# Performance work log

Hardware: AMD Instinct MI355X
Metric: run time of the kernel (lower is better)

## Reference

```python
import jax, jax.numpy as jnp
import numpy as np

B, N, F_IN, C_OUT = 128, 512, 2, 64
C_IN = F_IN + C_OUT           # 66, concat(input, state) feature dim
MLP_IN = (2 * 3 + 1) * C_IN   # order=2, support_len=3 -> 462


def _gcn(x, supports, W, b):
    """Diffusion conv: x [B,N,F]; for each support a, 2 diffusion orders."""
    outs = [x]
    for a in supports:
        x1 = jnp.einsum('bnf,nm->bmf', x, a)
        x2 = jnp.einsum('bnf,nm->bmf', x1, a)
        outs += [x1, x2]
    h = jnp.concatenate(outs, axis=2)  # [B, N, 7*F]
    return h @ W + b                   # Linear (dropout is eval-mode identity)


def setup_inputs() -> dict:
    key = jax.random.key(0)
    ks = jax.random.split(key, 12)
    return {
        'input': jax.random.normal(ks[0], (B, N, F_IN), dtype=jnp.float32),
        'state': jax.random.normal(ks[1], (B, N, C_OUT), dtype=jnp.float32),
        'A0':    jax.random.uniform(ks[2], (N, N), dtype=jnp.float32),
        'A1':    jax.random.uniform(ks[3], (N, N), dtype=jnp.float32),
        'nv1_1': jax.random.normal(ks[4], (N, 10), dtype=jnp.float32),
        'nv2_1': jax.random.normal(ks[5], (10, N), dtype=jnp.float32),
        'W1':    jax.random.normal(ks[6], (MLP_IN, 2 * C_OUT), dtype=jnp.float32) * 0.02,
        'b1':    jnp.zeros((2 * C_OUT,), dtype=jnp.float32),
        'nv1_2': jax.random.normal(ks[7], (N, 10), dtype=jnp.float32),
        'nv2_2': jax.random.normal(ks[8], (10, N), dtype=jnp.float32),
        'W2':    jax.random.normal(ks[9], (MLP_IN, C_OUT), dtype=jnp.float32) * 0.02,
        'b2':    jnp.zeros((C_OUT,), dtype=jnp.float32),
    }


def reference(input, state, A0, A1, nv1_1, nv2_1, W1, b1, nv1_2, nv2_2, W2, b2):
    c_out = state.shape[-1]
    # gcn_1: adaptive adjacency + diffusion conv, then sigmoid gating split into r,u
    adp1 = jax.nn.softmax(jax.nn.relu(nv1_1 @ nv2_1), axis=1)
    x = jnp.concatenate([input, state], axis=2)
    value = jax.nn.sigmoid(_gcn(x, [A0, A1, adp1], W1, b1))
    r, u = value[..., :c_out], value[..., c_out:]
    # gcn_2: candidate state
    adp2 = jax.nn.softmax(jax.nn.relu(nv1_2 @ nv2_2), axis=1)
    x2 = jnp.concatenate([input, r * state], axis=2)
    c = jnp.tanh(_gcn(x2, [A0, A1, adp2], W2, b2))
    return u * state + (1.0 - u) * c
```

## Files before the change

### kernel.cpp

```cpp
#include <hip/hip_runtime.h>
#include <math.h>

#define NN 512
#define BB 128
#define CIN 66
#define QQ (BB*CIN)
#define AN ((size_t)NN*NN)
#define HB 480
#define KTOT 480

typedef unsigned short ushort_t;
typedef __attribute__((ext_vector_type(8))) short short8;
typedef __attribute__((ext_vector_type(8))) unsigned short us8;
typedef __attribute__((ext_vector_type(4))) float f32x4;
typedef __attribute__((ext_vector_type(4))) unsigned short us4;

__device__ __forceinline__ ushort_t f2bf(float f) {
    unsigned u = __float_as_uint(f);
    u += 0x7FFF + ((u >> 16) & 1);
    return (ushort_t)(u >> 16);
}
__device__ __forceinline__ float bf2f(ushort_t h) {
    return __uint_as_float(((unsigned)h) << 16);
}
__device__ __forceinline__ void split_bf(float f, ushort_t& hi, ushort_t& lo) {
    hi = f2bf(f);
    lo = f2bf(f - bf2f(hi));
}
__device__ __forceinline__ void gload_lds16(const void* g, void* l) {
    __builtin_amdgcn_global_load_lds(
        (const __attribute__((address_space(1))) unsigned*)g,
        (__attribute__((address_space(3))) unsigned*)l, 16, 0, 0);
}

__global__ __launch_bounds__(512) void adp_kernel(const float* __restrict__ nv1,
                                                  const float* __restrict__ nv2,
                                                  float* __restrict__ adp) {
    int n = blockIdx.x;
    int m = threadIdx.x;
    float z = 0.f;
#pragma unroll
    for (int k = 0; k < 10; k++) z = fmaf(nv1[n * 10 + k], nv2[k * NN + m], z);
    z = fmaxf(z, 0.f);

    __shared__ float sred[8];
    int wid  = threadIdx.x >> 6;
    int lane = threadIdx.x & 63;

    float v = z;
#pragma unroll
    for (int off = 32; off; off >>= 1) v = fmaxf(v, __shfl_down(v, off, 64));
    if (lane == 0) sred[wid] = v;
    __syncthreads();
    float zmax = sred[0];
#pragma unroll
    for (int i = 1; i < 8; i++) zmax = fmaxf(zmax, sred[i]);

    float e = __expf(z - zmax);
    __syncthreads();
    v = e;
#pragma unroll
    for (int off = 32; off; off >>= 1) v += __shfl_down(v, off, 64);
    if (lane == 0) sred[wid] = v;
    __syncthreads();
    float tot = 0.f;
#pragma unroll
    for (int i = 0; i < 8; i++) tot += sred[i];

    adp[n * NN + m] = e / tot;
}

__global__ __launch_bounds__(256) void asplit_kernel(const float* __restrict__ A0,
                                                     const float* __restrict__ A1,
                                                     const float* __restrict__ P1,
                                                     const float* __restrict__ P2,
                                                     ushort_t* __restrict__ Ahi,
                                                     ushort_t* __restrict__ Alo) {
    __shared__ float t[32][33];
    int s = blockIdx.z;
    const float* src = (s == 0) ? A0 : (s == 1) ? A1 : (s == 2) ? P1 : P2;
    int m0 = blockIdx.x * 32, k0 = blockIdx.y * 32;
    int tx = threadIdx.x & 31, ty = threadIdx.x >> 5;
#pragma unroll
    for (int r = 0; r < 32; r += 8)
        t[ty + r][tx] = src[(size_t)(k0 + ty + r) * NN + m0 + tx];
    __syncthreads();
#pragma unroll
    for (int r = 0; r < 32; r += 8) {
        int m = m0 + ty + r, k = k0 + tx;
        float v = t[tx][ty + r];
        ushort_t h, l; split_bf(v, h, l);
        size_t o = ((size_t)s * NN + m) * NN + k;
        Ahi[o] = h; Alo[o] = l;
    }
}

template <int COUT>
__global__ __launch_bounds__(256) void wtprep_kernel(const float* __restrict__ W,
                                                     ushort_t* __restrict__ Wth,
                                                     ushort_t* __restrict__ Wtl) {
    int j = blockIdx.x;
    for (int k = threadIdx.x; k < KTOT; k += 256) {
        float v = (k < 462) ? W[(size_t)k * COUT + j] : 0.f;
        ushort_t h, l; split_bf(v, h, l);
        Wth[(size_t)j * KTOT + k] = h;
        Wtl[(size_t)j * KTOT + k] = l;
    }
}

__global__ __launch_bounds__(256) void buildx_kernel(const float* __restrict__ inp,
                                                     const float* __restrict__ st,
                                                     ushort_t* __restrict__ Hh,
                                                     ushort_t* __restrict__ Hl) {
    int b = blockIdx.y, n = blockIdx.x * 64 + (threadIdx.x & 63);
    int cg = threadIdx.x >> 6;
    size_t bn = (size_t)b * NN + n;
    for (int c = cg; c < CIN; c += 4) {
        float v = (c < 2) ? inp[bn * 2 + c] : st[bn * 64 + (c - 2)];
        ushort_t h, l; split_bf(v, h, l);
        Hh[((size_t)b * HB + c) * NN + n] = h;
        Hl[((size_t)b * HB + c) * NN + n] = l;
    }
}

template <int HOP>
__global__ __launch_bounds__(256) void diff_mfma(const ushort_t* __restrict__ Ahi,
                                                 const ushort_t* __restrict__ Alo,
                                                 ushort_t* Hh, ushort_t* Hl, int s2) {
    __shared__ ushort_t sAh[128 * 32];
    __shared__ ushort_t sAl[128 * 32];
    __shared__ ushort_t sXh[128 * 32];
    __shared__ ushort_t sXl[128 * 32];
    const int tid  = threadIdx.x;
    const int lane = tid & 63, w = tid >> 6;
    const int quad = lane >> 4, l15 = lane & 15;
    const int q0 = blockIdx.x * 128, m0 = blockIdx.y * 128;
    const int sz = blockIdx.z;
    const int sup = (sz < 2) ? sz : s2;
    const ushort_t* Ah = Ahi + (size_t)sup * AN;
    const ushort_t* Al = Alo + (size_t)sup * AN;
    const int roff_in = (HOP == 1) ? 0 : 66 + 132 * sz;
    const int wm = w & 1, wq = w >> 1;

    size_t aoff[2], xoff[2];
    int ldo[2];
#pragma unroll
    for (int p = 0; p < 2; p++) {
        int cid = p * 256 + tid;
        int row = cid >> 2, kk = (cid & 3) * 8;
        ldo[p]  = cid * 8;
        aoff[p] = (size_t)(m0 + row) * NN + kk;
        int q = q0 + row, b = q / 66, c = q - 66 * b;
        xoff[p] = ((size_t)b * HB + roff_in + c) * NN + kk;
    }

    f32x4 acc[4][4] = {};

    for (int k0 = 0; k0 < NN; k0 += 32) {
        __syncthreads();
#pragma unroll
        for (int p = 0; p < 2; p++) {
            gload_lds16(Ah + aoff[p] + k0, sAh + ldo[p]);
            gload_lds16(Al + aoff[p] + k0, sAl + ldo[p]);
            gload_lds16(Hh + xoff[p] + k0, sXh + ldo[p]);
            gload_lds16(Hl + xoff[p] + k0, sXl + ldo[p]);
        }
        __syncthreads();
        short8 ah[4], al[4], xh[4], xl[4];
#pragma unroll
        for (int t = 0; t < 4; t++) {
            int arow = wm * 64 + t * 16 + l15;
            int xrow = wq * 64 + t * 16 + l15;
            ah[t] = *(const short8*)&sAh[arow * 32 + quad * 8];
            al[t] = *(const short8*)&sAl[arow * 32 + quad * 8];
            xh[t] = *(const short8*)&sXh[xrow * 32 + quad * 8];
            xl[t] = *(const short8*)&sXl[xrow * 32 + quad * 8];
        }
#pragma unroll
        for (int mt = 0; mt < 4; mt++)
#pragma unroll
            for (int qt = 0; qt < 4; qt++) {
                acc[mt][qt] = __builtin_amdgcn_mfma_f32_16x16x32_bf16(ah[mt], xh[qt], acc[mt][qt], 0, 0, 0);
                acc[mt][qt] = __builtin_amdgcn_mfma_f32_16x16x32_bf16(ah[mt], xl[qt], acc[mt][qt], 0, 0, 0);
                acc[mt][qt] = __builtin_amdgcn_mfma_f32_16x16x32_bf16(al[mt], xh[qt], acc[mt][qt], 0, 0, 0);
                acc[mt][qt] = __builtin_amdgcn_mfma_f32_16x16x32_bf16(al[mt], xl[qt], acc[mt][qt], 0, 0, 0);
            }
    }

    const int rowo = (HOP == 1) ? 66 + 132 * sz : 132 + 132 * sz;
#pragma unroll
    for (int qt = 0; qt < 4; qt++) {
        int q = q0 + wq * 64 + qt * 16 + l15;
        int b = q / 66, c = q - 66 * b;
#pragma unroll
        for (int mt = 0; mt < 4; mt++) {
            int n = m0 + wm * 64 + mt * 16 + quad * 4;
            us4 h4, l4;
#pragma unroll
            for (int r = 0; r < 4; r++) {
                ushort_t h, l; split_bf(acc[mt][qt][r], h, l);
                h4[r] = h; l4[r] = l;
            }
            size_t ho = ((size_t)b * HB + rowo + c) * NN + n;
            *(us4*)&Hh[ho] = h4;
            *(us4*)&Hl[ho] = l4;
        }
    }
}

template <int COUT, int LAYER, int BM>
__global__ __launch_bounds__(256) void proj_mfma(const ushort_t* HhC, const ushort_t* HlC,
                                                 const ushort_t* __restrict__ Wth,
                                                 const ushort_t* __restrict__ Wtl,
                                                 const float* __restrict__ bias,
                                                 const float* __restrict__ state,
                                                 float* U,
                                                 ushort_t* Hhw, ushort_t* Hlw,
                                                 float* __restrict__ out) {
    __shared__ ushort_t sAh[BM * 32];
    __shared__ ushort_t sAl[BM * 32];
    __shared__ ushort_t sBh[COUT * 32];
    __shared__ ushort_t sBl[COUT * 32];
    constexpr int PB = COUT / 64;
    const int tid  = threadIdx.x;
    const int lane = tid & 63, w = tid >> 6;
    const int quad = lane >> 4, l15 = lane & 15;
    const int b = blockIdx.y, n0 = blockIdx.x * BM;
    const int wn = (COUT == 128) ? (w & 1) : w;
    const int wj = (COUT == 128) ? (w >> 1) : 0;
    const int kp = tid & 15, n8 = tid >> 4;

    size_t boff[PB]; int lB[PB];
#pragma unroll
    for (int p = 0; p < PB; p++) {
        int cid = p * 256 + tid;
        lB[p]   = cid * 8;
        boff[p] = (size_t)(cid >> 2) * KTOT + (cid & 3) * 8;
    }

    f32x4 acc[4][4] = {};

    for (int k0 = 0; k0 < KTOT; k0 += 32) {
        __syncthreads();
#pragma unroll
        for (int pass = 0; pass < BM / 128; pass++) {
            int np0 = (n8 + pass * 16) * 8;
            int kk  = k0 + 2 * kp;
            const ushort_t* sh = HhC + ((size_t)b * HB + kk) * NN + n0 + np0;
            const ushort_t* sl = HlC + ((size_t)b * HB + kk) * NN + n0 + np0;
            us8 h0 = *(const us8*)sh;
            us8 h1 = *(const us8*)(sh + NN);
            us8 l0 = *(const us8*)sl;
            us8 l1 = *(const us8*)(sl + NN);
            int g = kp >> 2, ko = (2 * kp) & 7;
#pragma unroll
            for (int j2 = 0; j2 < 8; j2++) {
                int n   = np0 + j2;
                int idx = n * 32 + ((g ^ ((n >> 1) & 3)) << 3) + ko;
                *(unsigned*)&sAh[idx] = (unsigned)h0[j2] | ((unsigned)h1[j2] << 16);
                *(unsigned*)&sAl[idx] = (unsigned)l0[j2] | ((unsigned)l1[j2] << 16);
            }
        }
#pragma unroll
        for (int p = 0; p < PB; p++) {
            gload_lds16(Wth + boff[p] + k0, sBh + lB[p]);
            gload_lds16(Wtl + boff[p] + k0, sBl + lB[p]);
        }
        __syncthreads();
        short8 ah[4], al[4], bh[4], bl[4];
#pragma unroll
        for (int t = 0; t < 4; t++) {
            int an  = wn * 64 + t * 16 + l15;
            int ago = (quad ^ ((an >> 1) & 3)) << 3;
            ah[t] = *(const short8*)&sAh[an * 32 + ago];
            al[t] = *(const short8*)&sAl[an * 32 + ago];
            int brow = wj * 64 + t * 16 + l15;
            bh[t] = *(const short8*)&sBh[brow * 32 + quad * 8];
            bl[t] = *(const short8*)&sBl[brow * 32 + quad * 8];
        }
#pragma unroll
        for (int nt = 0; nt < 4; nt++)
#pragma unroll
            for (int jt = 0; jt < 4; jt++) {
                acc[nt][jt] = __builtin_amdgcn_mfma_f32_16x16x32_bf16(ah[nt], bh[jt], acc[nt][jt], 0, 0, 0);
                acc[nt][jt] = __builtin_amdgcn_mfma_f32_16x16x32_bf16(ah[nt], bl[jt], acc[nt][jt], 0, 0, 0);
                acc[nt][jt] = __builtin_amdgcn_mfma_f32_16x16x32_bf16(al[nt], bh[jt], acc[nt][jt], 0, 0, 0);
                acc[nt][jt] = __builtin_amdgcn_mfma_f32_16x16x32_bf16(al[nt], bl[jt], acc[nt][jt], 0, 0, 0);
            }
    }

#pragma unroll
    for (int jt = 0; jt < 4; jt++) {
        int j = wj * 64 + jt * 16 + l15;
        float bj = bias[j];
#pragma unroll
        for (int nt = 0; nt < 4; nt++) {
            int nb = n0 + wn * 64 + nt * 16 + quad * 4;
            f32x4 z = acc[nt][jt];
#pragma unroll
            for (int r = 0; r < 4; r++) z[r] += bj;
            if (LAYER == 1) {
#pragma unroll
                for (int r = 0; r < 4; r++) z[r] = 1.f / (1.f + __expf(-z[r]));
                if (j < 64) {
                    us4 h4, l4;
#pragma unroll
                    for (int r = 0; r < 4; r++) {
                        float x2 = z[r] * state[((size_t)b * NN + nb + r) * 64 + j];
                        ushort_t h, l; split_bf(x2, h, l);
                        h4[r] = h; l4[r] = l;
                    }
                    size_t ho = ((size_t)b * HB + 2 + j) * NN + nb;
                    *(us4*)&Hhw[ho] = h4;
                    *(us4*)&Hlw[ho] = l4;
                } else {
                    *(f32x4*)&U[((size_t)b * 64 + j - 64) * NN + nb] = z;
                }
            } else {
                f32x4 u4 = *(const f32x4*)&U[((size_t)b * 64 + j) * NN + nb];
#pragma unroll
                for (int r = 0; r < 4; r++) {
                    float c = tanhf(z[r]);
                    float s = state[((size_t)b * NN + nb + r) * 64 + j];
                    out[((size_t)b * NN + nb + r) * 64 + j] = u4[r] * s + (1.f - u4[r]) * c;
                }
            }
        }
    }
}

extern "C" void kernel_launch(void* const* d_in, const int* in_sizes, int n_in,
                              void* d_out, int out_size, void* d_ws, size_t ws_size,
                              hipStream_t stream) {
    const float* input = (const float*)d_in[0];
    const float* state = (const float*)d_in[1];
    const float* A0    = (const float*)d_in[2];
    const float* A1    = (const float*)d_in[3];
    const float* nv1_1 = (const float*)d_in[4];
    const float* nv2_1 = (const float*)d_in[5];
    const float* W1    = (const float*)d_in[6];
    const float* b1    = (const float*)d_in[7];
    const float* nv1_2 = (const float*)d_in[8];
    const float* nv2_2 = (const float*)d_in[9];
    const float* W2    = (const float*)d_in[10];
    const float* b2    = (const float*)d_in[11];
    float* out = (float*)d_out;

    char* p = (char*)d_ws;
    auto alloc = [&](size_t bytes) { void* r = (void*)p; p += (bytes + 255) & ~(size_t)255; return r; };
    float*    ADP1 = (float*)alloc(AN * 4);
    float*    ADP2 = (float*)alloc(AN * 4);
    ushort_t* Ahi  = (ushort_t*)alloc(4 * AN * 2);
    ushort_t* Alo  = (ushort_t*)alloc(4 * AN * 2);
    ushort_t* Hh   = (ushort_t*)alloc((size_t)BB * HB * NN * 2);
    ushort_t* Hl   = (ushort_t*)alloc((size_t)BB * HB * NN * 2);
    ushort_t* Wt1h = (ushort_t*)alloc((size_t)128 * KTOT * 2);
    ushort_t* Wt1l = (ushort_t*)alloc((size_t)128 * KTOT * 2);
    ushort_t* Wt2h = (ushort_t*)alloc((size_t)64 * KTOT * 2);
    ushort_t* Wt2l = (ushort_t*)alloc((size_t)64 * KTOT * 2);
    float*    U    = (float*)alloc((size_t)BB * 64 * NN * 4);

    adp_kernel<<<NN, NN, 0, stream>>>(nv1_1, nv2_1, ADP1);
    adp_kernel<<<NN, NN, 0, stream>>>(nv1_2, nv2_2, ADP2);
    asplit_kernel<<<dim3(16, 16, 4), 256, 0, stream>>>(A0, A1, ADP1, ADP2, Ahi, Alo);
    wtprep_kernel<128><<<128, 256, 0, stream>>>(W1, Wt1h, Wt1l);
    wtprep_kernel<64><<<64, 256, 0, stream>>>(W2, Wt2h, Wt2l);
    buildx_kernel<<<dim3(8, BB), 256, 0, stream>>>(input, state, Hh, Hl);

    dim3 gd(QQ / 128, NN / 128, 3);
    diff_mfma<1><<<gd, 256, 0, stream>>>(Ahi, Alo, Hh, Hl, 2);
    diff_mfma<2><<<gd, 256, 0, stream>>>(Ahi, Alo, Hh, Hl, 2);
    proj_mfma<128, 1, 128><<<dim3(NN / 128, BB), 256, 0, stream>>>(Hh, Hl, Wt1h, Wt1l, b1, state,
                                                                   U, Hh, Hl, nullptr);
    diff_mfma<1><<<gd, 256, 0, stream>>>(Ahi, Alo, Hh, Hl, 3);
    diff_mfma<2><<<gd, 256, 0, stream>>>(Ahi, Alo, Hh, Hl, 3);
    proj_mfma<64, 2, 256><<<dim3(NN / 256, BB), 256, 0, stream>>>(Hh, Hl, Wt2h, Wt2l, b2, state,
                                                                  U, nullptr, nullptr, out);
}
```

Measured before the change: 486.1 us.

## Pre-pack adjacency into MFMA fragment order and double-buffer X tiles

The adjacency prep kernel now writes the hi/lo bf16 matrices in a fragment-major layout, so each lane can load its MFMA A-operand directly from global memory with one 16-byte read, skipping LDS. The X operand tiles are double-buffered in LDS, and the next k-tile is prefetched while the current one is computed, which drops one barrier per iteration. The aim is to cut LDS traffic and synchronisation and overlap loads with MFMA work. In exchange, A fragments come from global/L2 per wave with no LDS sharing, so latency may be exposed because there is no register prefetch.

```diff
diff --git a/kernel.cpp b/kernel.cpp
--- a/kernel.cpp
+++ b/kernel.cpp
@@ -90,7 +90,9 @@
         int m = m0 + ty + r, k = k0 + tx;
         float v = t[tx][ty + r];
         ushort_t h, l; split_bf(v, h, l);
-        size_t o = ((size_t)s * NN + m) * NN + k;
+        int mt = m >> 4, l15 = m & 15;
+        int kt = k >> 5, quad = (k >> 3) & 3, j = k & 7;
+        size_t o = ((((size_t)s * 16 + kt) * 32 + mt) * 64 + quad * 16 + l15) * 8 + j;
         Ahi[o] = h; Alo[o] = l;
     }
 }
@@ -124,57 +126,62 @@
 }
 
 template <int HOP>
-__global__ __launch_bounds__(256) void diff_mfma(const ushort_t* __restrict__ Ahi,
-                                                 const ushort_t* __restrict__ Alo,
+__global__ __launch_bounds__(256) void diff_mfma(const ushort_t* __restrict__ Aph,
+                                                 const ushort_t* __restrict__ Apl,
                                                  ushort_t* Hh, ushort_t* Hl, int s2) {
-    __shared__ ushort_t sAh[128 * 32];
-    __shared__ ushort_t sAl[128 * 32];
-    __shared__ ushort_t sXh[128 * 32];
-    __shared__ ushort_t sXl[128 * 32];
+    __shared__ ushort_t sXh[2][128 * 32];
+    __shared__ ushort_t sXl[2][128 * 32];
     const int tid  = threadIdx.x;
     const int lane = tid & 63, w = tid >> 6;
     const int quad = lane >> 4, l15 = lane & 15;
     const int q0 = blockIdx.x * 128, m0 = blockIdx.y * 128;
     const int sz = blockIdx.z;
     const int sup = (sz < 2) ? sz : s2;
-    const ushort_t* Ah = Ahi + (size_t)sup * AN;
-    const ushort_t* Al = Alo + (size_t)sup * AN;
     const int roff_in = (HOP == 1) ? 0 : 66 + 132 * sz;
     const int wm = w & 1, wq = w >> 1;
 
-    size_t aoff[2], xoff[2];
+    size_t xoff[2];
     int ldo[2];
 #pragma unroll
     for (int p = 0; p < 2; p++) {
         int cid = p * 256 + tid;
         int row = cid >> 2, kk = (cid & 3) * 8;
         ldo[p]  = cid * 8;
-        aoff[p] = (size_t)(m0 + row) * NN + kk;
         int q = q0 + row, b = q / 66, c = q - 66 * b;
         xoff[p] = ((size_t)b * HB + roff_in + c) * NN + kk;
     }
 
     f32x4 acc[4][4] = {};
 
-    for (int k0 = 0; k0 < NN; k0 += 32) {
-        __syncthreads();
-#pragma unroll
-        for (int p = 0; p < 2; p++) {
-            gload_lds16(Ah + aoff[p] + k0, sAh + ldo[p]);
-            gload_lds16(Al + aoff[p] + k0, sAl + ldo[p]);
-            gload_lds16(Hh + xoff[p] + k0, sXh + ldo[p]);
-            gload_lds16(Hl + xoff[p] + k0, sXl + ldo[p]);
-        }
-        __syncthreads();
+#pragma unroll
+    for (int p = 0; p < 2; p++) {
+        gload_lds16(Hh + xoff[p], &sXh[0][ldo[p]]);
+        gload_lds16(Hl + xoff[p], &sXl[0][ldo[p]]);
+    }
+    __syncthreads();
+
+    const size_t abase = (size_t)sup * 16 * 32 * 512;
+    const int mtg0 = (m0 >> 4) + wm * 4;
+
+    for (int kt = 0; kt < 16; kt++) {
+        const int cur = kt & 1;
+        if (kt < 15) {
+            const int k1 = (kt + 1) * 32;
+#pragma unroll
+            for (int p = 0; p < 2; p++) {
+                gload_lds16(Hh + xoff[p] + k1, &sXh[cur ^ 1][ldo[p]]);
+                gload_lds16(Hl + xoff[p] + k1, &sXl[cur ^ 1][ldo[p]]);
+            }
+        }
         short8 ah[4], al[4], xh[4], xl[4];
 #pragma unroll
         for (int t = 0; t < 4; t++) {
-            int arow = wm * 64 + t * 16 + l15;
+            size_t fo = (abase + ((size_t)kt * 32 + mtg0 + t) * 512) + (size_t)lane * 8;
+            ah[t] = *(const short8*)&Aph[fo];
+            al[t] = *(const short8*)&Apl[fo];
             int xrow = wq * 64 + t * 16 + l15;
-            ah[t] = *(const short8*)&sAh[arow * 32 + quad * 8];
-            al[t] = *(const short8*)&sAl[arow * 32 + quad * 8];
-            xh[t] = *(const short8*)&sXh[xrow * 32 + quad * 8];
-            xl[t] = *(const short8*)&sXl[xrow * 32 + quad * 8];
+            xh[t] = *(const short8*)&sXh[cur][xrow * 32 + quad * 8];
+            xl[t] = *(const short8*)&sXl[cur][xrow * 32 + quad * 8];
         }
 #pragma unroll
         for (int mt = 0; mt < 4; mt++)
@@ -185,6 +192,7 @@
                 acc[mt][qt] = __builtin_amdgcn_mfma_f32_16x16x32_bf16(al[mt], xh[qt], acc[mt][qt], 0, 0, 0);
                 acc[mt][qt] = __builtin_amdgcn_mfma_f32_16x16x32_bf16(al[mt], xl[qt], acc[mt][qt], 0, 0, 0);
             }
+        __syncthreads();
     }
 
     const int rowo = (HOP == 1) ? 66 + 132 * sz : 132 + 132 * sz;
```

After: 538.2 us. 10.7% more time.
